# Kernel tuning notes

Hardware: AMD Instinct MI355X
Metric: run time of the kernel (lower is better)

The kernel has to match this reference:

```python
import jax, jax.numpy as jnp
import numpy as np

P = 16          # patch_size
E = 16          # num_experts
K = 4           # top-k
NOISE_STD = 1.0 / E


def setup_inputs() -> dict:
    key = jax.random.key(0)
    k0, k1, k2, k3, k4, k5 = jax.random.split(key, 6)
    B, C, H, W = 8, 128, 512, 512
    FD = 512
    n_patches = (H // P) * (W // P)  # 1024
    x = jax.random.normal(k0, (B, C, H, W), jnp.float32)
    freq_emb = jax.random.normal(k1, (B, FD), jnp.float32)
    # torch does randn_like(logits) * noise_std inside forward; pre-scaled here for determinism
    noise = jax.random.normal(k2, (B, n_patches, E), jnp.float32) * NOISE_STD
    conv_w = jax.random.normal(k3, (E, C, P, P), jnp.float32) * 0.02
    conv_b = jax.random.normal(k4, (E,), jnp.float32) * 0.02
    freq_w = jax.random.normal(k5, (E, FD), jnp.float32) * 0.05
    return {"x": x, "freq_emb": freq_emb, "noise": noise,
            "conv_w": conv_w, "conv_b": conv_b, "freq_w": freq_w}


def reference(x, freq_emb, noise, conv_w, conv_b, freq_w):
    B, C, H, W = x.shape
    h, w = H // P, W // P
    n = h * w
    # patchify conv (kernel=stride=patch_size) == per-patch GEMM
    patches = x.reshape(B, C, h, P, w, P)                      # [B,C,h,P,w,P]
    spatial = jnp.einsum('bchpwq,ecpq->bhwe', patches, conv_w) + conv_b
    spatial = spatial.reshape(B, n, E)                         # b (h w) e
    freq = (freq_emb @ freq_w.T)[:, None, :]                   # [B,1,E]
    logits = spatial + freq                                    # [B,n,E]
    noisy_logits = logits + noise
    gating_scores = jax.nn.softmax(noisy_logits, axis=-1)
    top_k_values, top_k_indices = jax.lax.top_k(gating_scores, K)  # [B,n,K]
    gates = jnp.zeros_like(logits).at[
        jnp.arange(B)[:, None, None],
        jnp.arange(n)[None, :, None],
        top_k_indices,
    ].set(top_k_values)
    aux_loss = jnp.float32(0.0)  # eval path: no importance/load losses
    return gates, top_k_indices, top_k_values, aux_loss
```

## Files before the change

### kernel.cpp

```cpp
#include <hip/hip_runtime.h>

#define B_ 8
#define C_ 128
#define HW_ 512
#define PS 16
#define E_ 16
#define NP 1024
#define FD 512
#define CH_STRIDE (HW_ * HW_)


__global__ void freq_kernel(const float* __restrict__ femb,
                            const float* __restrict__ fw,
                            float* __restrict__ freqf,
                            float* __restrict__ out) {
    int t = threadIdx.x;
    if (t == 0) out[196608] = 0.0f;
    if (t < 128) {
        int b = t >> 4, e = t & 15;
        const float* fe = femb + b * FD;
        const float* w  = fw + e * FD;
        double s = 0.0;
        for (int i = 0; i < FD; ++i)
            s = fma((double)fe[i], (double)w[i], s);
        freqf[t] = (float)s;
    }
}

#define MAC4(XF, WF)                                        \
    acc = __fadd_rn(acc, __fmul_rn((XF).x, (WF).x));        \
    acc = __fadd_rn(acc, __fmul_rn((XF).y, (WF).y));        \
    acc = __fadd_rn(acc, __fmul_rn((XF).z, (WF).z));        \
    acc = __fadd_rn(acc, __fmul_rn((XF).w, (WF).w));

#define GLOAD_LDS(GSRC, LDST)                                                  \
  __builtin_amdgcn_global_load_lds(                                            \
      (const __attribute__((address_space(1))) void*)(GSRC),                   \
      (__attribute__((address_space(3))) void*)(LDST), 16, 0, 0)

#define LROW 260

__global__ __launch_bounds__(256, 2) void patch_route_kernel(
    const float* __restrict__ x,
    const float* __restrict__ noise,
    const float* __restrict__ conv_w,
    const float* __restrict__ conv_b,
    const float* __restrict__ freqf,
    float* __restrict__ out) {

  __shared__ float xs[2][16][LROW];
  __shared__ float ws[2][16][LROW];
  __shared__ float slg[16][16];

  const int blk = blockIdx.x;
  const int b   = blk >> 6;
  const int pg  = blk & 63;
  const int t   = threadIdx.x;
  const int lp  = t >> 4;
  const int e   = t & 15;
  const int lp16 = lp * 16;
  const int patch = pg * 16 + lp;
  const int pi = pg >> 1;
  const int wv   = t >> 6;
  const int lane = t & 63;

  const float* xblk = x + (size_t)b * (C_ * CH_STRIDE)
                        + (size_t)(pi * PS) * HW_ + (pg & 1) * 256;

  {
    const float* xc = xblk;
    const float* wc = conv_w;
    #pragma unroll
    for (int r = 0; r < 4; ++r) {
      const int p = wv * 4 + r;
      GLOAD_LDS(xc + p * HW_ + lane * 4, &xs[0][p][0]);
    }
    #pragma unroll
    for (int r = 0; r < 4; ++r) {
      const int ee = wv * 4 + r;
      GLOAD_LDS(wc + (size_t)ee * 32768 + lane * 4, &ws[0][ee][0]);
    }
  }

  float acc = 0.0f;
  for (int c = 0; c < C_; ++c) {
    const int cur = c & 1;
    if (c + 1 < C_) {
      const int nb = cur ^ 1;
      const float* xc = xblk + (size_t)(c + 1) * CH_STRIDE;
      const float* wc = conv_w + (c + 1) * 256;
      #pragma unroll
      for (int r = 0; r < 4; ++r) {
        const int p = wv * 4 + r;
        GLOAD_LDS(xc + p * HW_ + lane * 4, &xs[nb][p][0]);
      }
      #pragma unroll
      for (int r = 0; r < 4; ++r) {
        const int ee = wv * 4 + r;
        GLOAD_LDS(wc + (size_t)ee * 32768 + lane * 4, &ws[nb][ee][0]);
      }
      asm volatile("s_waitcnt vmcnt(8)" ::: "memory");
    } else {
      asm volatile("s_waitcnt vmcnt(0)" ::: "memory");
    }
    __builtin_amdgcn_s_barrier();
    __builtin_amdgcn_sched_barrier(0);

    #pragma unroll
    for (int p = 0; p < 16; ++p) {
      const float4 x0 = *reinterpret_cast<const float4*>(&xs[cur][p][lp16 +  0]);
      const float4 x1 = *reinterpret_cast<const float4*>(&xs[cur][p][lp16 +  4]);
      const float4 x2 = *reinterpret_cast<const float4*>(&xs[cur][p][lp16 +  8]);
      const float4 x3 = *reinterpret_cast<const float4*>(&xs[cur][p][lp16 + 12]);
      const float4 w0 = *reinterpret_cast<const float4*>(&ws[cur][e][p * 16 +  0]);
      const float4 w1 = *reinterpret_cast<const float4*>(&ws[cur][e][p * 16 +  4]);
      const float4 w2 = *reinterpret_cast<const float4*>(&ws[cur][e][p * 16 +  8]);
      const float4 w3 = *reinterpret_cast<const float4*>(&ws[cur][e][p * 16 + 12]);
      MAC4(x0, w0);
      MAC4(x1, w1);
      MAC4(x2, w2);
      MAC4(x3, w3);
    }

    __builtin_amdgcn_sched_barrier(0);
    __builtin_amdgcn_s_barrier();
  }

  float lg = __fadd_rn(acc, conv_b[e]);
  lg = __fadd_rn(lg, freqf[b * 16 + e]);
  lg = __fadd_rn(lg, noise[((size_t)b * NP + patch) * 16 + e]);

  slg[lp][e] = lg;
  __syncthreads();

  if (t < 16) {
    const int pp = t;
    const int pat = pg * 16 + pp;
    float v[16];
    #pragma unroll
    for (int i = 0; i < 16; ++i) v[i] = slg[pp][i];

    float m = v[0];
    #pragma unroll
    for (int i = 1; i < 16; ++i) m = fmaxf(m, v[i]);

    float ex[16];
    #pragma unroll
    for (int i = 0; i < 16; ++i) ex[i] = expf(v[i] - m);

    float r[8];
    #pragma unroll
    for (int j = 0; j < 8; ++j) r[j] = __fadd_rn(ex[j], ex[j + 8]);
    float d0 = __fadd_rn(__fadd_rn(r[0], r[1]), __fadd_rn(r[2], r[3]));
    float d1 = __fadd_rn(__fadd_rn(r[4], r[5]), __fadd_rn(r[6], r[7]));
    float den = __fadd_rn(d0, d1);

    float s[16];
    #pragma unroll
    for (int i = 0; i < 16; ++i) s[i] = ex[i] / den;

    unsigned mask = 0;
    int bidx[4]; float bval[4];
    #pragma unroll
    for (int j = 0; j < 4; ++j) {
      int bi = 0; float bv = -1.0f;
      #pragma unroll
      for (int i = 0; i < 16; ++i) {
        if (!((mask >> i) & 1u) && s[i] > bv) { bv = s[i]; bi = i; }
      }
      mask |= 1u << bi;
      bidx[j] = bi; bval[j] = bv;
    }

    const size_t po = (size_t)b * NP + pat;
    float* gout = out + po * 16;
    float* iout = out + 131072 + po * 4;
    float* vout = out + 163840 + po * 4;
    #pragma unroll
    for (int j = 0; j < 4; ++j) {
      iout[j] = (float)bidx[j];
      vout[j] = bval[j];
    }
    #pragma unroll
    for (int i = 0; i < 16; ++i)
      gout[i] = ((mask >> i) & 1u) ? s[i] : 0.0f;
  }
}

extern "C" void kernel_launch(void* const* d_in, const int* in_sizes, int n_in,
                              void* d_out, int out_size, void* d_ws, size_t ws_size,
                              hipStream_t stream) {
  const float* x     = (const float*)d_in[0];
  const float* femb  = (const float*)d_in[1];
  const float* noise = (const float*)d_in[2];
  const float* cw    = (const float*)d_in[3];
  const float* cb    = (const float*)d_in[4];
  const float* fw    = (const float*)d_in[5];
  float* out = (float*)d_out;
  float* freqf = (float*)d_ws;

  hipLaunchKernelGGL(freq_kernel, dim3(1), dim3(128), 0, stream,
                     femb, fw, freqf, out);
  hipLaunchKernelGGL(patch_route_kernel, dim3(512), dim3(256), 0, stream,
                     x, noise, cw, cb, freqf, out);
}
```

Before: 360.4 us.

## Triple-buffer channel pipeline and process full patch row per 512-thread block

Each block now covers a whole row of 32 patches with 512 threads, so every conv weight tile loaded into LDS is shared by twice as many patches, and the grid halves to 256 blocks. The LDS buffering goes from double to triple, prefetching two channels ahead, which allows the trailing barrier per channel to be dropped. The aim is less redundant weight traffic and fewer barriers. In exchange, LDS use per block rises and only 256 blocks are launched, which may leave some compute units idle on a large GPU.

New measurement: 420.5 us. 1.17x slower.

```diff
diff --git a/kernel.cpp b/kernel.cpp
--- a/kernel.cpp
+++ b/kernel.cpp
@@ -8,6 +8,7 @@
 #define NP 1024
 #define FD 512
 #define CH_STRIDE (HW_ * HW_)
+#define WROW 260
 
 
 __global__ void freq_kernel(const float* __restrict__ femb,
@@ -38,9 +39,7 @@
       (const __attribute__((address_space(1))) void*)(GSRC),                   \
       (__attribute__((address_space(3))) void*)(LDST), 16, 0, 0)
 
-#define LROW 260
-
-__global__ __launch_bounds__(256, 2) void patch_route_kernel(
+__global__ __launch_bounds__(512, 1) void patch_route_kernel(
     const float* __restrict__ x,
     const float* __restrict__ noise,
     const float* __restrict__ conv_w,
@@ -48,63 +47,56 @@
     const float* __restrict__ freqf,
     float* __restrict__ out) {
 
-  __shared__ float xs[2][16][LROW];
-  __shared__ float ws[2][16][LROW];
-  __shared__ float slg[16][16];
+  __shared__ float xs[3][16][512];
+  __shared__ float ws[3][16][WROW];
+  __shared__ float slg[32][16];
 
-  const int blk = blockIdx.x;
-  const int b   = blk >> 6;
-  const int pg  = blk & 63;
-  const int t   = threadIdx.x;
-  const int lp  = t >> 4;
-  const int e   = t & 15;
+  const int blk  = blockIdx.x;
+  const int b    = blk >> 5;
+  const int prow = blk & 31;
+  const int t    = threadIdx.x;
+  const int lp   = t >> 4;
+  const int e    = t & 15;
   const int lp16 = lp * 16;
-  const int patch = pg * 16 + lp;
-  const int pi = pg >> 1;
   const int wv   = t >> 6;
   const int lane = t & 63;
 
   const float* xblk = x + (size_t)b * (C_ * CH_STRIDE)
-                        + (size_t)(pi * PS) * HW_ + (pg & 1) * 256;
+                        + (size_t)(prow * PS) * HW_;
 
-  {
-    const float* xc = xblk;
-    const float* wc = conv_w;
-    #pragma unroll
-    for (int r = 0; r < 4; ++r) {
-      const int p = wv * 4 + r;
-      GLOAD_LDS(xc + p * HW_ + lane * 4, &xs[0][p][0]);
-    }
-    #pragma unroll
-    for (int r = 0; r < 4; ++r) {
-      const int ee = wv * 4 + r;
-      GLOAD_LDS(wc + (size_t)ee * 32768 + lane * 4, &ws[0][ee][0]);
-    }
+#define STAGE(CH, BUF)                                                         \
+  {                                                                            \
+    const float* xc = xblk + (size_t)(CH) * CH_STRIDE;                         \
+    const float* wc = conv_w + (CH) * 256;                                     \
+    _Pragma("unroll")                                                          \
+    for (int r = 0; r < 4; ++r) {                                              \
+      const int g = wv * 4 + r;                                     \
+      const int p = g >> 1, half = g & 1;                                      \
+      GLOAD_LDS(xc + p * HW_ + half * 256 + lane * 4,                          \
+                &xs[BUF][p][half * 256]);                                      \
+    }                                                                          \
+    _Pragma("unroll")                                                          \
+    for (int r = 0; r < 2; ++r) {                                              \
+      const int ee = wv * 2 + r;                                    \
+      GLOAD_LDS(wc + (size_t)ee * 32768 + lane * 4, &ws[BUF][ee][0]);          \
+    }                                                                          \
   }
+
+  STAGE(0, 0)
+  STAGE(1, 1)
 
   float acc = 0.0f;
   for (int c = 0; c < C_; ++c) {
-    const int cur = c & 1;
-    if (c + 1 < C_) {
-      const int nb = cur ^ 1;
-      const float* xc = xblk + (size_t)(c + 1) * CH_STRIDE;
-      const float* wc = conv_w + (c + 1) * 256;
-      #pragma unroll
-      for (int r = 0; r < 4; ++r) {
-        const int p = wv * 4 + r;
-        GLOAD_LDS(xc + p * HW_ + lane * 4, &xs[nb][p][0]);
-      }
-      #pragma unroll
-      for (int r = 0; r < 4; ++r) {
-        const int ee = wv * 4 + r;
-        GLOAD_LDS(wc + (size_t)ee * 32768 + lane * 4, &ws[nb][ee][0]);
-      }
-      asm volatile("s_waitcnt vmcnt(8)" ::: "memory");
+    const int cur = c % 3;
+    if (c < C_ - 1) {
+      asm volatile("s_waitcnt vmcnt(6)" ::: "memory");
     } else {
       asm volatile("s_waitcnt vmcnt(0)" ::: "memory");
     }
     __builtin_amdgcn_s_barrier();
     __builtin_amdgcn_sched_barrier(0);
+
+    if (c + 2 < C_) STAGE(c + 2, (c + 2) % 3)
 
     #pragma unroll
     for (int p = 0; p < 16; ++p) {
@@ -121,11 +113,10 @@
       MAC4(x2, w2);
       MAC4(x3, w3);
     }
-
     __builtin_amdgcn_sched_barrier(0);
-    __builtin_amdgcn_s_barrier();
   }
 
+  const int patch = prow * 32 + lp;
   float lg = __fadd_rn(acc, conv_b[e]);
   lg = __fadd_rn(lg, freqf[b * 16 + e]);
   lg = __fadd_rn(lg, noise[((size_t)b * NP + patch) * 16 + e]);
@@ -133,9 +124,9 @@
   slg[lp][e] = lg;
   __syncthreads();
 
-  if (t < 16) {
+  if (t < 32) {
     const int pp = t;
-    const int pat = pg * 16 + pp;
+    const int pat = prow * 32 + pp;
     float v[16];
     #pragma unroll
     for (int i = 0; i < 16; ++i) v[i] = slg[pp][i];
@@ -201,6 +192,6 @@
 
   hipLaunchKernelGGL(freq_kernel, dim3(1), dim3(128), 0, stream,
                      femb, fw, freqf, out);
-  hipLaunchKernelGGL(patch_route_kernel, dim3(512), dim3(256), 0, stream,
+  hipLaunchKernelGGL(patch_route_kernel, dim3(256), dim3(512), 0, stream,
                      x, noise, cw, cb, freqf, out);
 }
```
